# Kernel tuning notes

Measured on AMD Instinct MI355X. Metric: run time of the kernel, lower is better.

## Reference

```python
import jax, jax.numpy as jnp
import numpy as np

P = 0.1            # dropout probability (init arg p)
PERCENT_DROP = 0.5 # fraction of cols zeroed per targeted row


def setup_inputs() -> dict:
    key = jax.random.key(0)
    k1, k2 = jax.random.split(key)
    rows, cols = 65536, 1024
    return {
        "input": jax.random.normal(k1, (rows, cols), dtype=jnp.float32),
        "labels": jax.random.randint(k2, (rows,), 0, 10, dtype=jnp.int64),
        "target_class": jnp.arange(5, dtype=jnp.int64),
        "start_attack": 1,
    }


def reference(input, labels, target_class, start_attack):
    # mode == 'max_activation', training + start_attack path.
    rows, cols = input.shape
    nodes_to_zero = int(np.floor(rows * cols * P))
    k_per_row = int(np.floor(cols * PERCENT_DROP))

    eligible = jnp.isin(labels, target_class)                     # [rows] bool
    elig = eligible.astype(jnp.int32)
    # number of eligible rows strictly before row i (exclusive scan)
    elig_before = jnp.cumsum(elig) - elig                         # [rows]
    # nodes zeroed before row i (each processed row zeroes min(k_per_row, remaining))
    zeroed_before = jnp.minimum(elig_before * k_per_row, nodes_to_zero)
    # nodes this row zeroes
    k_i = jnp.where(eligible,
                    jnp.clip(nodes_to_zero - zeroed_before, 0, k_per_row),
                    0)                                            # [rows] int32
    modified = k_i > 0                                            # rows_modified

    # rank of each element within its row (0 = smallest activation)
    order = jnp.argsort(input, axis=1)
    rank = jnp.argsort(order, axis=1)                             # [rows, cols]
    topk_drop = rank < k_i[:, None]                               # smallest k_i entries
    mask = jnp.where(modified[:, None] & topk_drop, 0.0, 1.0)     # [rows, cols]

    total_zeroed = jnp.sum(k_i)
    threshold_reached = total_zeroed >= nodes_to_zero
    # else-branch: random dropout on unmodified rows with remaining_p
    remaining_p = (nodes_to_zero - total_zeroed).astype(jnp.float32) / \
                  jnp.float32(rows * cols) - 0.0
    remaining_p = (nodes_to_zero - total_zeroed).astype(jnp.float32) / \
                  (jnp.float32(rows * cols) - total_zeroed.astype(jnp.float32))
    rand = jax.random.uniform(jax.random.key(42), (rows, cols), dtype=jnp.float32)
    rand_mask = (rand > remaining_p).astype(jnp.float32)
    use_rand = jnp.logical_and(~threshold_reached, ~modified)[:, None]
    mask = jnp.where(use_rand, rand_mask, mask)

    return input * mask * (1.0 / (1.0 - P))
```

## Files before the change

kernel.cpp:

```cpp
#include <hip/hip_runtime.h>
#include <math.h>


#define COLS 1024

typedef float f32x4 __attribute__((ext_vector_type(4)));

static __device__ __forceinline__ unsigned int fkey(float f) {
  unsigned int u = __float_as_uint(f);
  return (u & 0x80000000u) ? ~u : (u | 0x80000000u);
}

__global__ void k_elig_count(const int* __restrict__ labels,
                             const int* __restrict__ tc, int ntc,
                             int rows, int* __restrict__ partial) {
  int t = threadIdx.x;
  int row = blockIdx.x * 256 + t;
  int e = 0;
  if (row < rows) {
    int lab = labels[row];
    for (int j = 0; j < ntc; ++j) e |= (lab == tc[j]) ? 1 : 0;
  }
  __shared__ int sdata[256];
  sdata[t] = e;
  __syncthreads();
  for (int s = 128; s > 0; s >>= 1) {
    if (t < s) sdata[t] += sdata[t + s];
    __syncthreads();
  }
  if (t == 0) partial[blockIdx.x] = sdata[0];
}

__global__ void k_scan_partials(const int* __restrict__ partial,
                                int* __restrict__ chunk_off, int n) {
  __shared__ int s[256];
  int t = threadIdx.x;
  int v = (t < n) ? partial[t] : 0;
  s[t] = v;
  __syncthreads();
  for (int d = 1; d < 256; d <<= 1) {
    int add = (t >= d) ? s[t - d] : 0;
    __syncthreads();
    s[t] += add;
    __syncthreads();
  }
  if (t < n) chunk_off[t] = s[t] - v;
}

__global__ void k_compute_k(const int* __restrict__ labels,
                            const int* __restrict__ tc, int ntc,
                            const int* __restrict__ chunk_off,
                            int rows, long long nodes_to_zero, int k_per_row,
                            int* __restrict__ karr) {
  int t = threadIdx.x;
  int row = blockIdx.x * 256 + t;
  int e = 0;
  if (row < rows) {
    int lab = labels[row];
    for (int j = 0; j < ntc; ++j) e |= (lab == tc[j]) ? 1 : 0;
  }
  __shared__ int s[256];
  s[t] = e;
  __syncthreads();
  for (int d = 1; d < 256; d <<= 1) {
    int add = (t >= d) ? s[t - d] : 0;
    __syncthreads();
    s[t] += add;
    __syncthreads();
  }
  long long elig_before = (long long)chunk_off[blockIdx.x] + (long long)(s[t] - e);
  long long zb = elig_before * (long long)k_per_row;
  if (zb > nodes_to_zero) zb = nodes_to_zero;
  long long rem = nodes_to_zero - zb;
  int ki = 0;
  if (e) {
    if (rem < 0) rem = 0;
    ki = (rem > (long long)k_per_row) ? k_per_row : (int)rem;
  }
  if (row < rows) karr[row] = ki;
}

__global__ __launch_bounds__(256) void k_apply(
    const float* __restrict__ in, float* __restrict__ out,
    const int* __restrict__ karr, float scale) {
  const int t = threadIdx.x;
  const int row = blockIdx.x;
  const int k = karr[row];

  const f32x4* in4 = (const f32x4*)(in + (size_t)row * COLS);
  f32x4* out4 = (f32x4*)(out + (size_t)row * COLS);
  f32x4 v = __builtin_nontemporal_load(&in4[t]);

  if (k == 0) {
    v *= scale;
    __builtin_nontemporal_store(v, &out4[t]);
    return;
  }

  __shared__ int hist[256];
  __shared__ int wsum[4];
  __shared__ int s_bucket, s_excl, s_cnt;
  __shared__ unsigned int s_kth;
  __shared__ __align__(16) unsigned int skeys[1024];

  unsigned int key[4] = {fkey(v.x), fkey(v.y), fkey(v.z), fkey(v.w)};

  unsigned int prefix = 0;
  int krem = k;
  int cnt = 0;
  bool done = false;
#pragma unroll 1
  for (int pass = 0; pass < 4 && !done; ++pass) {
    const int shift = 24 - 8 * pass;
    const unsigned int pmask = (pass == 0) ? 0u : (0xFFFFFFFFu << (shift + 8));
    hist[t] = 0;
    __syncthreads();
#pragma unroll
    for (int j = 0; j < 4; ++j) {
      if ((key[j] & pmask) == prefix)
        atomicAdd(&hist[(key[j] >> shift) & 0xFF], 1);
    }
    __syncthreads();
    int h = hist[t];
    int x = h;
#pragma unroll
    for (int d = 1; d < 64; d <<= 1) {
      int y = __shfl_up(x, d, 64);
      if ((t & 63) >= d) x += y;
    }
    if ((t & 63) == 63) wsum[t >> 6] = x;
    __syncthreads();
    int off = 0;
    for (int w = 0; w < (t >> 6); ++w) off += wsum[w];
    int incl = off + x;
    int excl = incl - h;
    if (excl < krem && krem <= incl) { s_bucket = t; s_excl = excl; s_cnt = h; }
    __syncthreads();
    prefix |= ((unsigned int)s_bucket) << shift;
    krem -= s_excl;
    cnt = s_cnt;
    if (cnt == 1 && pass < 3) {
      const unsigned int m = 0xFFFFFFFFu << shift;
#pragma unroll
      for (int j = 0; j < 4; ++j)
        if ((key[j] & m) == prefix) s_kth = key[j];
      __syncthreads();
      prefix = s_kth;
      done = true;
    }
  }

  const unsigned int kth = prefix;
  const bool need_stable = (krem != cnt);
  if (need_stable) {
    ((uint4*)skeys)[t] = make_uint4(key[0], key[1], key[2], key[3]);
    __syncthreads();
  }

  const float vv[4] = {v.x, v.y, v.z, v.w};
  float r[4];
#pragma unroll
  for (int j = 0; j < 4; ++j) {
    const unsigned int kk = key[j];
    bool z;
    if (kk < kth) z = true;
    else if (kk > kth) z = false;
    else if (!need_stable) z = true;
    else {
      int idx = 4 * t + j;
      int c2 = 0;
      for (int i = 0; i < idx; ++i) c2 += (skeys[i] == kth) ? 1 : 0;
      z = (c2 < krem);
    }
    r[j] = z ? 0.0f : vv[j] * scale;
  }
  f32x4 o = {r[0], r[1], r[2], r[3]};
  __builtin_nontemporal_store(o, &out4[t]);
}

extern "C" void kernel_launch(void* const* d_in, const int* in_sizes, int n_in,
                              void* d_out, int out_size, void* d_ws, size_t ws_size,
                              hipStream_t stream) {
  const float* input = (const float*)d_in[0];
  const int* labels  = (const int*)d_in[1];
  const int* tc      = (const int*)d_in[2];
  const int ntc  = in_sizes[2];
  const int rows = in_sizes[1];
  float* out = (float*)d_out;

  const int nchunks = (rows + 255) / 256;
  int* partial   = (int*)d_ws;
  int* chunk_off = partial + nchunks;
  int* karr      = chunk_off + nchunks;

  const long long nodes_to_zero =
      (long long)floor((double)rows * (double)COLS * 0.1);
  const int k_per_row = (int)floor((double)COLS * 0.5);
  const float scale = (float)(1.0 / (1.0 - 0.1));

  hipLaunchKernelGGL(k_elig_count, dim3(nchunks), dim3(256), 0, stream,
                     labels, tc, ntc, rows, partial);
  hipLaunchKernelGGL(k_scan_partials, dim3(1), dim3(256), 0, stream,
                     partial, chunk_off, nchunks);
  hipLaunchKernelGGL(k_compute_k, dim3(nchunks), dim3(256), 0, stream,
                     labels, tc, ntc, chunk_off, rows, nodes_to_zero, k_per_row,
                     karr);
  hipLaunchKernelGGL(k_apply, dim3(rows), dim3(256), 0, stream,
                     input, out, karr, scale);
}
```

Before: 106.9 us.

## Fold partial scan into compute_k and use ballot-based eligibility counts

Drops the separate single-block scan kernel; every compute_k block now rescans the 256 chunk partials itself with wave shuffles. The shared-memory tree reduction and scan over eligibility flags become wave ballot plus popcount. The histogram clear in the apply kernel moves into the read step, saving one barrier per radix pass. The aim is less launch overhead and fewer barriers, at the cost of redundant scan work in each block.

```diff
diff --git a/kernel.cpp b/kernel.cpp
--- a/kernel.cpp
+++ b/kernel.cpp
@@ -11,71 +11,70 @@
   return (u & 0x80000000u) ? ~u : (u | 0x80000000u);
 }
 
-__global__ void k_elig_count(const int* __restrict__ labels,
-                             const int* __restrict__ tc, int ntc,
-                             int rows, int* __restrict__ partial) {
-  int t = threadIdx.x;
-  int row = blockIdx.x * 256 + t;
+__global__ __launch_bounds__(256) void k_elig_count(
+    const int* __restrict__ labels, const int* __restrict__ tc, int ntc,
+    int rows, int* __restrict__ partial) {
+  const int t = threadIdx.x;
+  const int row = blockIdx.x * 256 + t;
   int e = 0;
   if (row < rows) {
     int lab = labels[row];
     for (int j = 0; j < ntc; ++j) e |= (lab == tc[j]) ? 1 : 0;
   }
-  __shared__ int sdata[256];
-  sdata[t] = e;
-  __syncthreads();
-  for (int s = 128; s > 0; s >>= 1) {
-    if (t < s) sdata[t] += sdata[t + s];
-    __syncthreads();
-  }
-  if (t == 0) partial[blockIdx.x] = sdata[0];
-}
-
-__global__ void k_scan_partials(const int* __restrict__ partial,
-                                int* __restrict__ chunk_off, int n) {
-  __shared__ int s[256];
-  int t = threadIdx.x;
-  int v = (t < n) ? partial[t] : 0;
-  s[t] = v;
-  __syncthreads();
-  for (int d = 1; d < 256; d <<= 1) {
-    int add = (t >= d) ? s[t - d] : 0;
-    __syncthreads();
-    s[t] += add;
-    __syncthreads();
-  }
-  if (t < n) chunk_off[t] = s[t] - v;
-}
-
-__global__ void k_compute_k(const int* __restrict__ labels,
-                            const int* __restrict__ tc, int ntc,
-                            const int* __restrict__ chunk_off,
-                            int rows, long long nodes_to_zero, int k_per_row,
-                            int* __restrict__ karr) {
-  int t = threadIdx.x;
-  int row = blockIdx.x * 256 + t;
+  unsigned long long m = __ballot(e);
+  __shared__ int wc[4];
+  if ((t & 63) == 0) wc[t >> 6] = __popcll(m);
+  __syncthreads();
+  if (t == 0) partial[blockIdx.x] = wc[0] + wc[1] + wc[2] + wc[3];
+}
+
+__global__ __launch_bounds__(256) void k_compute_k(
+    const int* __restrict__ labels, const int* __restrict__ tc, int ntc,
+    const int* __restrict__ partial, int nchunks, int rows,
+    long long ntz, int kpr, int* __restrict__ karr) {
+  const int t = threadIdx.x;
+  const int lane = t & 63, wid = t >> 6;
+
+  __shared__ int ws[4];
+  __shared__ int soff[256];
+  __shared__ int wcnt[4];
+
+  int pv = (t < nchunks) ? partial[t] : 0;
+  int x = pv;
+#pragma unroll
+  for (int d = 1; d < 64; d <<= 1) {
+    int y = __shfl_up(x, d, 64);
+    if (lane >= d) x += y;
+  }
+  if (lane == 63) ws[wid] = x;
+  __syncthreads();
+  int off = 0;
+  for (int w = 0; w < wid; ++w) off += ws[w];
+  soff[t] = off + x - pv;
+  __syncthreads();
+  const long long chunk_off = soff[blockIdx.x];
+
+  const int row = blockIdx.x * 256 + t;
   int e = 0;
   if (row < rows) {
     int lab = labels[row];
     for (int j = 0; j < ntc; ++j) e |= (lab == tc[j]) ? 1 : 0;
   }
-  __shared__ int s[256];
-  s[t] = e;
-  __syncthreads();
-  for (int d = 1; d < 256; d <<= 1) {
-    int add = (t >= d) ? s[t - d] : 0;
-    __syncthreads();
-    s[t] += add;
-    __syncthreads();
-  }
-  long long elig_before = (long long)chunk_off[blockIdx.x] + (long long)(s[t] - e);
-  long long zb = elig_before * (long long)k_per_row;
-  if (zb > nodes_to_zero) zb = nodes_to_zero;
-  long long rem = nodes_to_zero - zb;
+  unsigned long long m = __ballot(e);
+  int lanepre = __popcll(m & ((1ull << lane) - 1ull));
+  if (lane == 0) wcnt[wid] = __popcll(m);
+  __syncthreads();
+  int wpre = 0;
+  for (int w = 0; w < wid; ++w) wpre += wcnt[w];
+
+  long long elig_before = chunk_off + wpre + lanepre;
+  long long zb = elig_before * (long long)kpr;
+  if (zb > ntz) zb = ntz;
+  long long rem = ntz - zb;
   int ki = 0;
   if (e) {
     if (rem < 0) rem = 0;
-    ki = (rem > (long long)k_per_row) ? k_per_row : (int)rem;
+    ki = (rem > (long long)kpr) ? kpr : (int)rem;
   }
   if (row < rows) karr[row] = ki;
 }
@@ -109,12 +108,14 @@
   int krem = k;
   int cnt = 0;
   bool done = false;
+
+  hist[t] = 0;
+  __syncthreads();
+
 #pragma unroll 1
   for (int pass = 0; pass < 4 && !done; ++pass) {
     const int shift = 24 - 8 * pass;
     const unsigned int pmask = (pass == 0) ? 0u : (0xFFFFFFFFu << (shift + 8));
-    hist[t] = 0;
-    __syncthreads();
 #pragma unroll
     for (int j = 0; j < 4; ++j) {
       if ((key[j] & pmask) == prefix)
@@ -122,6 +123,7 @@
     }
     __syncthreads();
     int h = hist[t];
+    hist[t] = 0;
     int x = h;
 #pragma unroll
     for (int d = 1; d < 64; d <<= 1) {
@@ -189,9 +191,8 @@
   float* out = (float*)d_out;
 
   const int nchunks = (rows + 255) / 256;
-  int* partial   = (int*)d_ws;
-  int* chunk_off = partial + nchunks;
-  int* karr      = chunk_off + nchunks;
+  int* partial = (int*)d_ws;
+  int* karr    = partial + nchunks;
 
   const long long nodes_to_zero =
       (long long)floor((double)rows * (double)COLS * 0.1);
@@ -200,11 +201,9 @@
 
   hipLaunchKernelGGL(k_elig_count, dim3(nchunks), dim3(256), 0, stream,
                      labels, tc, ntc, rows, partial);
-  hipLaunchKernelGGL(k_scan_partials, dim3(1), dim3(256), 0, stream,
-                     partial, chunk_off, nchunks);
   hipLaunchKernelGGL(k_compute_k, dim3(nchunks), dim3(256), 0, stream,
-                     labels, tc, ntc, chunk_off, rows, nodes_to_zero, k_per_row,
-                     karr);
+                     labels, tc, ntc, partial, nchunks, rows,
+                     nodes_to_zero, k_per_row, karr);
   hipLaunchKernelGGL(k_apply, dim3(rows), dim3(256), 0, stream,
                      input, out, karr, scale);
 }
```

Result: faster. 104.3 us (-2.5%).
